# Optimization experiments

Hardware: AMD Instinct MI355X
Metric: run time of the kernel (lower is better)

## Reference

```python
import jax, jax.numpy as jnp
import numpy as np

N_NODES = 100000
D_FEAT = 128
N_GATHER = 1600000
N_MACRO = 50000


def setup_inputs() -> dict:
    key = jax.random.key(0)
    k1, k2, k3 = jax.random.split(key, 3)
    node_feature = jax.random.normal(k1, (N_NODES, D_FEAT), dtype=jnp.float32)
    batch_node_ids = jax.random.randint(k2, (N_GATHER,), 0, N_NODES, dtype=jnp.int64 if jax.config.jax_enable_x64 else jnp.int32)
    batch_macro_node_ids = jnp.sort(jax.random.randint(k3, (N_GATHER,), 0, N_MACRO, dtype=jnp.int64 if jax.config.jax_enable_x64 else jnp.int32))
    return {
        "node_feature": node_feature,
        "batch_node_ids": batch_node_ids,
        "batch_macro_node_ids": batch_macro_node_ids,
        "num_macro_nodes": N_MACRO,
    }


def reference(node_feature, batch_node_ids, batch_macro_node_ids, num_macro_nodes):
    # gather: [n_gather, d]
    gathered = node_feature[batch_node_ids]
    # scatter-mean by segment id -> [num_macro_nodes, d]
    sums = jax.ops.segment_sum(gathered, batch_macro_node_ids, num_segments=num_macro_nodes)
    counts = jax.ops.segment_sum(
        jnp.ones((batch_macro_node_ids.shape[0],), dtype=node_feature.dtype),
        batch_macro_node_ids, num_segments=num_macro_nodes)
    # empty segments stay 0 (matches torch_scatter 'mean' behavior)
    return sums / jnp.maximum(counts, 1.0)[:, None]
```

## Files before the change

kernel.cpp:

```cpp
#include <hip/hip_runtime.h>

#define D_FEAT 128
#define MAX_CHUNK 1024

__global__ __launch_bounds__(256)
void prep_kernel(const float* __restrict__ feat,
                 unsigned char* __restrict__ tab, float* __restrict__ scales,
                 int n_nodes, int qb,
                 const int* __restrict__ mids, int n_gather,
                 int num_macro, int* __restrict__ offsets) {
    if ((int)blockIdx.x < qb) {
        const int wave = threadIdx.x >> 6;
        const int lane = threadIdx.x & 63;
        const int row  = blockIdx.x * 4 + wave;
        if (row >= n_nodes) return;
        const float2 v = ((const float2*)feat)[(size_t)row * 64 + lane];
        float a = fmaxf(fabsf(v.x), fabsf(v.y));
        #pragma unroll
        for (int d = 1; d <= 32; d <<= 1) a = fmaxf(a, __shfl_xor(a, d, 64));
        const float inv = (a > 0.f) ? (127.f / a) : 0.f;
        const int q0 = (int)rintf(v.x * inv);
        const int q1 = (int)rintf(v.y * inv);
        const unsigned short p =
            (unsigned short)((q0 & 0xFF) | ((q1 & 0xFF) << 8));
        ((unsigned short*)tab)[(size_t)row * 64 + lane] = p;
        if (lane == 0) scales[row] = a * (1.f / 127.f);
    } else {
        const int i = ((int)blockIdx.x - qb) * 256 + (int)threadIdx.x;
        if (i >= n_gather) return;
        const int cur  = mids[i];
        const int prev = (i == 0) ? -1 : mids[i - 1];
        for (int m = prev + 1; m <= cur; ++m) offsets[m] = i;
        if (i == n_gather - 1) {
            for (int m = cur + 1; m <= num_macro; ++m) offsets[m] = n_gather;
        }
    }
}

__global__ __launch_bounds__(256)
void pool_wave_i8_v3_kernel(const unsigned char* __restrict__ tab,
                            const float* __restrict__ scales,
                            const int* __restrict__ nids,
                            const int* __restrict__ offsets,
                            float* __restrict__ out, int num_macro) {
    const int wave = threadIdx.x >> 6;
    const int m    = blockIdx.x * 4 + wave;
    if (m >= num_macro) return;

    const int lane = threadIdx.x & 63;
    const int slot = lane >> 4;
    const int co   = (lane & 15) << 3;

    const int start = offsets[m];
    const int cnt   = offsets[m + 1] - start;

    float acc[8];
    #pragma unroll
    for (int f = 0; f < 8; ++f) acc[f] = 0.f;

    for (int b0 = 0; b0 < cnt; b0 += 64) {
        const int rem = min(cnt - b0, 64);
        const int my = nids[start + b0 + ((lane < rem) ? lane : rem - 1)];
        float scz    = scales[my];
        if (lane >= rem) scz = 0.f;

        for (int k = 0; k < rem; k += 16) {
            uint2 w[4];
            float s[4];
            #pragma unroll
            for (int j = 0; j < 4; ++j) {
                const int src = k + (j << 2) + slot;
                const int idx = __shfl(my, src, 64);
                s[j] = __shfl(scz, src, 64);
                w[j] = *(const uint2*)(tab + (((unsigned)idx << 7) + (unsigned)co));
            }
            #pragma unroll
            for (int j = 0; j < 4; ++j) {
                const unsigned lo = w[j].x;
                const unsigned hi = w[j].y;
                acc[0] += s[j] * (float)(signed char)( lo         & 0xFF);
                acc[1] += s[j] * (float)(signed char)((lo >> 8)   & 0xFF);
                acc[2] += s[j] * (float)(signed char)((lo >> 16)  & 0xFF);
                acc[3] += s[j] * (float)(signed char)( lo >> 24);
                acc[4] += s[j] * (float)(signed char)( hi         & 0xFF);
                acc[5] += s[j] * (float)(signed char)((hi >> 8)   & 0xFF);
                acc[6] += s[j] * (float)(signed char)((hi >> 16)  & 0xFF);
                acc[7] += s[j] * (float)(signed char)( hi >> 24);
            }
        }
    }

    #pragma unroll
    for (int f = 0; f < 8; ++f) {
        acc[f] += __shfl_xor(acc[f], 16, 64);
        acc[f] += __shfl_xor(acc[f], 32, 64);
    }

    if (slot == 0) {
        const float inv = (cnt > 0) ? (1.0f / (float)cnt) : 0.0f;
        float* dst = out + (size_t)m * D_FEAT + co;
        *(float4*)(dst)     = make_float4(acc[0] * inv, acc[1] * inv,
                                          acc[2] * inv, acc[3] * inv);
        *(float4*)(dst + 4) = make_float4(acc[4] * inv, acc[5] * inv,
                                          acc[6] * inv, acc[7] * inv);
    }
}

__global__ __launch_bounds__(256)
void pool_mean_fp32_kernel(const float* __restrict__ feat,
                           const int* __restrict__ nids,
                           const int* __restrict__ offsets,
                           float* __restrict__ out) {
    const int m    = blockIdx.x;
    const int tid  = threadIdx.x;
    const int g    = tid >> 5;
    const int c4   = (tid & 31) << 2;

    const int start = offsets[m];
    const int cnt   = offsets[m + 1] - start;

    __shared__ int   s_idx[MAX_CHUNK];
    __shared__ float red[8][D_FEAT];

    float4 acc = make_float4(0.f, 0.f, 0.f, 0.f);
    for (int base = 0; base < cnt; base += MAX_CHUNK) {
        const int chunk = min(cnt - base, MAX_CHUNK);
        for (int t = tid; t < chunk; t += 256) s_idx[t] = nids[start + base + t];
        __syncthreads();
        int r = g;
        for (; r + 24 < chunk; r += 32) {
            const float4 v0 = *(const float4*)(feat + (size_t)s_idx[r]      * D_FEAT + c4);
            const float4 v1 = *(const float4*)(feat + (size_t)s_idx[r + 8]  * D_FEAT + c4);
            const float4 v2 = *(const float4*)(feat + (size_t)s_idx[r + 16] * D_FEAT + c4);
            const float4 v3 = *(const float4*)(feat + (size_t)s_idx[r + 24] * D_FEAT + c4);
            acc.x += v0.x + v1.x + v2.x + v3.x;
            acc.y += v0.y + v1.y + v2.y + v3.y;
            acc.z += v0.z + v1.z + v2.z + v3.z;
            acc.w += v0.w + v1.w + v2.w + v3.w;
        }
        for (; r < chunk; r += 8) {
            const float4 v = *(const float4*)(feat + (size_t)s_idx[r] * D_FEAT + c4);
            acc.x += v.x; acc.y += v.y; acc.z += v.z; acc.w += v.w;
        }
        __syncthreads();
    }

    red[g][c4 + 0] = acc.x;
    red[g][c4 + 1] = acc.y;
    red[g][c4 + 2] = acc.z;
    red[g][c4 + 3] = acc.w;
    __syncthreads();

    if (tid < D_FEAT) {
        float s = 0.f;
        #pragma unroll
        for (int k = 0; k < 8; ++k) s += red[k][tid];
        const float inv = (cnt > 0) ? (1.0f / (float)cnt) : 0.0f;
        out[(size_t)m * D_FEAT + tid] = s * inv;
    }
}

__global__ __launch_bounds__(256)
void seg_offsets_kernel(const int* __restrict__ mids, int n_gather,
                        int num_macro, int* __restrict__ offsets) {
    const int i = blockIdx.x * blockDim.x + threadIdx.x;
    if (i >= n_gather) return;
    const int cur  = mids[i];
    const int prev = (i == 0) ? -1 : mids[i - 1];
    for (int m = prev + 1; m <= cur; ++m) offsets[m] = i;
    if (i == n_gather - 1) {
        for (int m = cur + 1; m <= num_macro; ++m) offsets[m] = n_gather;
    }
}

extern "C" void kernel_launch(void* const* d_in, const int* in_sizes, int n_in,
                              void* d_out, int out_size, void* d_ws, size_t ws_size,
                              hipStream_t stream) {
    const float* feat = (const float*)d_in[0];
    const int*   nids = (const int*)d_in[1];
    const int*   mids = (const int*)d_in[2];
    float*       out  = (float*)d_out;

    const int n_gather  = in_sizes[1];
    const int num_macro = out_size / D_FEAT;
    const int n_nodes   = in_sizes[0] / D_FEAT;

    int* offsets = (int*)d_ws;
    const size_t off_bytes   = ((size_t)(num_macro + 1) * sizeof(int) + 255) & ~(size_t)255;
    const size_t scale_bytes = ((size_t)n_nodes * sizeof(float) + 255) & ~(size_t)255;
    const size_t tab_bytes   = (size_t)n_nodes * D_FEAT;
    const bool   use_i8      = (off_bytes + scale_bytes + tab_bytes) <= ws_size;

    if (use_i8) {
        float*         scales = (float*)((char*)d_ws + off_bytes);
        unsigned char* tab    = (unsigned char*)((char*)d_ws + off_bytes + scale_bytes);

        const int qb = (n_nodes + 3) / 4;
        const int ob = (n_gather + 255) / 256;
        prep_kernel<<<qb + ob, 256, 0, stream>>>(
            feat, tab, scales, n_nodes, qb, mids, n_gather, num_macro, offsets);

        pool_wave_i8_v3_kernel<<<(num_macro + 3) / 4, 256, 0, stream>>>(
            tab, scales, nids, offsets, out, num_macro);
    } else {
        seg_offsets_kernel<<<(n_gather + 255) / 256, 256, 0, stream>>>(
            mids, n_gather, num_macro, offsets);
        pool_mean_fp32_kernel<<<num_macro, 256, 0, stream>>>(feat, nids, offsets, out);
    }
}
```

Before: 144.1 us.

## Split int8 feature table into column slices and pre-gather per-element scales

Stores the quantized node table as four 32-column slices, so each pool block touches only one 3.2MB slice at a time, which is meant to improve L2 locality for random gathers. Adds a separate kernel that gathers per-element scales into a contiguous array, and restructures pooling so each wave handles one segment's slice with 16 elements per iteration. The cost is an extra launch, a 6.4MB scale array write and read, and each nid being read four times, once per slice block.

```diff
diff --git a/kernel.cpp b/kernel.cpp
--- a/kernel.cpp
+++ b/kernel.cpp
@@ -1,6 +1,8 @@
 #include <hip/hip_runtime.h>
 
 #define D_FEAT 128
+#define NSLICE 4
+#define SLICE_COLS 32
 #define MAX_CHUNK 1024
 
 __global__ __launch_bounds__(256)
@@ -23,7 +25,9 @@
         const int q1 = (int)rintf(v.y * inv);
         const unsigned short p =
             (unsigned short)((q0 & 0xFF) | ((q1 & 0xFF) << 8));
-        ((unsigned short*)tab)[(size_t)row * 64 + lane] = p;
+        const size_t sliceBytes = (size_t)n_nodes * SLICE_COLS;
+        ((unsigned short*)(tab + (size_t)(lane >> 4) * sliceBytes
+                               + (size_t)row * SLICE_COLS))[lane & 15] = p;
         if (lane == 0) scales[row] = a * (1.f / 127.f);
     } else {
         const int i = ((int)blockIdx.x - qb) * 256 + (int)threadIdx.x;
@@ -38,18 +42,32 @@
 }
 
 __global__ __launch_bounds__(256)
-void pool_wave_i8_v3_kernel(const unsigned char* __restrict__ tab,
-                            const float* __restrict__ scales,
-                            const int* __restrict__ nids,
-                            const int* __restrict__ offsets,
-                            float* __restrict__ out, int num_macro) {
-    const int wave = threadIdx.x >> 6;
-    const int m    = blockIdx.x * 4 + wave;
+void sc_gather_kernel(const float* __restrict__ scales,
+                      const int* __restrict__ nids,
+                      float* __restrict__ sc_g, int n_gather) {
+    const int i = blockIdx.x * 256 + threadIdx.x;
+    if (i < n_gather) sc_g[i] = scales[nids[i]];
+}
+
+__global__ __launch_bounds__(256)
+void pool_slice_i8_kernel(const unsigned char* __restrict__ tab,
+                          const float* __restrict__ sc_g,
+                          const int* __restrict__ nids,
+                          const int* __restrict__ offsets,
+                          float* __restrict__ out, int num_macro, int n_nodes) {
+    const int wave  = threadIdx.x >> 6;
+    const int lane  = threadIdx.x & 63;
+    const int x     = (int)blockIdx.x & 7;
+    const int slice = x & 3;
+    const int sub   = x >> 2;
+    const int m     = ((int)blockIdx.x >> 3) * 8 + wave * 2 + sub;
     if (m >= num_macro) return;
 
-    const int lane = threadIdx.x & 63;
-    const int slot = lane >> 4;
-    const int co   = (lane & 15) << 3;
+    const unsigned char* sl =
+        tab + (size_t)slice * ((size_t)n_nodes * SLICE_COLS);
+
+    const int e  = lane >> 2;
+    const int q8 = (lane & 3) << 3;
 
     const int start = offsets[m];
     const int cnt   = offsets[m + 1] - start;
@@ -58,47 +76,55 @@
     #pragma unroll
     for (int f = 0; f < 8; ++f) acc[f] = 0.f;
 
-    for (int b0 = 0; b0 < cnt; b0 += 64) {
-        const int rem = min(cnt - b0, 64);
-        const int my = nids[start + b0 + ((lane < rem) ? lane : rem - 1)];
-        float scz    = scales[my];
-        if (lane >= rem) scz = 0.f;
-
-        for (int k = 0; k < rem; k += 16) {
-            uint2 w[4];
-            float s[4];
-            #pragma unroll
-            for (int j = 0; j < 4; ++j) {
-                const int src = k + (j << 2) + slot;
-                const int idx = __shfl(my, src, 64);
-                s[j] = __shfl(scz, src, 64);
-                w[j] = *(const uint2*)(tab + (((unsigned)idx << 7) + (unsigned)co));
-            }
-            #pragma unroll
-            for (int j = 0; j < 4; ++j) {
-                const unsigned lo = w[j].x;
-                const unsigned hi = w[j].y;
-                acc[0] += s[j] * (float)(signed char)( lo         & 0xFF);
-                acc[1] += s[j] * (float)(signed char)((lo >> 8)   & 0xFF);
-                acc[2] += s[j] * (float)(signed char)((lo >> 16)  & 0xFF);
-                acc[3] += s[j] * (float)(signed char)( lo >> 24);
-                acc[4] += s[j] * (float)(signed char)( hi         & 0xFF);
-                acc[5] += s[j] * (float)(signed char)((hi >> 8)   & 0xFF);
-                acc[6] += s[j] * (float)(signed char)((hi >> 16)  & 0xFF);
-                acc[7] += s[j] * (float)(signed char)( hi >> 24);
-            }
-        }
+    int k = 0;
+    for (; k + 32 <= cnt; k += 32) {
+        uint2 w[2]; float s[2];
+        #pragma unroll
+        for (int j = 0; j < 2; ++j) {
+            const int g = start + k + j * 16 + e;
+            const int n = nids[g];
+            s[j] = sc_g[g];
+            w[j] = *(const uint2*)(sl + ((size_t)n << 5) + q8);
+        }
+        #pragma unroll
+        for (int j = 0; j < 2; ++j) {
+            acc[0] += s[j] * (float)(signed char)( w[j].x        & 0xFF);
+            acc[1] += s[j] * (float)(signed char)((w[j].x >> 8)  & 0xFF);
+            acc[2] += s[j] * (float)(signed char)((w[j].x >> 16) & 0xFF);
+            acc[3] += s[j] * (float)(signed char)( w[j].x >> 24);
+            acc[4] += s[j] * (float)(signed char)( w[j].y        & 0xFF);
+            acc[5] += s[j] * (float)(signed char)((w[j].y >> 8)  & 0xFF);
+            acc[6] += s[j] * (float)(signed char)((w[j].y >> 16) & 0xFF);
+            acc[7] += s[j] * (float)(signed char)( w[j].y >> 24);
+        }
+    }
+    for (; k < cnt; k += 16) {
+        const int idx = k + e;
+        const int g   = start + ((idx < cnt) ? idx : cnt - 1);
+        const int n   = nids[g];
+        const float s = (idx < cnt) ? sc_g[g] : 0.f;
+        const uint2 w = *(const uint2*)(sl + ((size_t)n << 5) + q8);
+        acc[0] += s * (float)(signed char)( w.x        & 0xFF);
+        acc[1] += s * (float)(signed char)((w.x >> 8)  & 0xFF);
+        acc[2] += s * (float)(signed char)((w.x >> 16) & 0xFF);
+        acc[3] += s * (float)(signed char)( w.x >> 24);
+        acc[4] += s * (float)(signed char)( w.y        & 0xFF);
+        acc[5] += s * (float)(signed char)((w.y >> 8)  & 0xFF);
+        acc[6] += s * (float)(signed char)((w.y >> 16) & 0xFF);
+        acc[7] += s * (float)(signed char)( w.y >> 24);
     }
 
     #pragma unroll
     for (int f = 0; f < 8; ++f) {
+        acc[f] += __shfl_xor(acc[f], 4, 64);
+        acc[f] += __shfl_xor(acc[f], 8, 64);
         acc[f] += __shfl_xor(acc[f], 16, 64);
         acc[f] += __shfl_xor(acc[f], 32, 64);
     }
 
-    if (slot == 0) {
+    if (lane < 4) {
         const float inv = (cnt > 0) ? (1.0f / (float)cnt) : 0.0f;
-        float* dst = out + (size_t)m * D_FEAT + co;
+        float* dst = out + (size_t)m * D_FEAT + slice * SLICE_COLS + (lane << 3);
         *(float4*)(dst)     = make_float4(acc[0] * inv, acc[1] * inv,
                                           acc[2] * inv, acc[3] * inv);
         *(float4*)(dst + 4) = make_float4(acc[4] * inv, acc[5] * inv,
@@ -188,20 +214,28 @@
     int* offsets = (int*)d_ws;
     const size_t off_bytes   = ((size_t)(num_macro + 1) * sizeof(int) + 255) & ~(size_t)255;
     const size_t scale_bytes = ((size_t)n_nodes * sizeof(float) + 255) & ~(size_t)255;
+    const size_t scg_bytes   = ((size_t)n_gather * sizeof(float) + 255) & ~(size_t)255;
     const size_t tab_bytes   = (size_t)n_nodes * D_FEAT;
-    const bool   use_i8      = (off_bytes + scale_bytes + tab_bytes) <= ws_size;
+    const bool   use_i8      =
+        (off_bytes + scale_bytes + scg_bytes + tab_bytes) <= ws_size;
 
     if (use_i8) {
         float*         scales = (float*)((char*)d_ws + off_bytes);
-        unsigned char* tab    = (unsigned char*)((char*)d_ws + off_bytes + scale_bytes);
+        float*         sc_g   = (float*)((char*)d_ws + off_bytes + scale_bytes);
+        unsigned char* tab    =
+            (unsigned char*)((char*)d_ws + off_bytes + scale_bytes + scg_bytes);
 
         const int qb = (n_nodes + 3) / 4;
         const int ob = (n_gather + 255) / 256;
         prep_kernel<<<qb + ob, 256, 0, stream>>>(
             feat, tab, scales, n_nodes, qb, mids, n_gather, num_macro, offsets);
 
-        pool_wave_i8_v3_kernel<<<(num_macro + 3) / 4, 256, 0, stream>>>(
-            tab, scales, nids, offsets, out, num_macro);
+        sc_gather_kernel<<<(n_gather + 255) / 256, 256, 0, stream>>>(
+            scales, nids, sc_g, n_gather);
+
+        const int mblocks = ((num_macro + 7) / 8) * 8;
+        pool_slice_i8_kernel<<<mblocks, 256, 0, stream>>>(
+            tab, sc_g, nids, offsets, out, num_macro, n_nodes);
     } else {
         seg_offsets_kernel<<<(n_gather + 255) / 256, 256, 0, stream>>>(
             mids, n_gather, num_macro, offsets);
```

Result: slower. 192.5 us (+33.6%).
